# Performance work log

Measured on AMD Instinct MI355X. Metric: run time of the kernel, lower is better.

Reference implementation:

```python
import jax, jax.numpy as jnp
import numpy as np

MODEL_DIM = 256
HEADS = 8
LN_EPS = 1e-5


def layer_norm(x, gamma, beta):
    mu = jnp.mean(x, axis=-1, keepdims=True)
    var = jnp.var(x, axis=-1, keepdims=True)
    return (x - mu) * jax.lax.rsqrt(var + LN_EPS) * gamma + beta


def setup_inputs() -> dict:
    key = jax.random.key(0)
    ks = jax.random.split(key, 4)
    bs, n, d, h = 16, 1024, MODEL_DIM, HEADS
    scale = 1.0 / np.sqrt(d)
    x = jax.random.normal(ks[0], (bs, n, d), dtype=jnp.float32)
    Wq = jax.random.normal(ks[1], (d * h, d), dtype=jnp.float32) * scale
    Wk = jax.random.normal(ks[2], (d * h, d), dtype=jnp.float32) * scale
    Wv = jax.random.normal(ks[3], (d, d * h), dtype=jnp.float32) * (1.0 / np.sqrt(d * h))
    gamma = jnp.ones((d,), dtype=jnp.float32)
    beta = jnp.zeros((d,), dtype=jnp.float32)
    return {"x": x, "Wq": Wq, "Wk": Wk, "Wv": Wv, "gamma": gamma, "beta": beta}


def reference(x, Wq, Wk, Wv, gamma, beta):
    bs, n, d = x.shape
    h = HEADS
    # pre-norm
    xn = layer_norm(x, gamma, beta)
    # q, k: (bs, n, h, d) -> (bs, h, n, d); torch Linear: y = x @ W.T
    q = (xn @ Wq.T).reshape(bs, n, h, d).transpose(0, 2, 1, 3)
    k = (xn @ Wk.T).reshape(bs, n, h, d).transpose(0, 2, 1, 3)
    scores = jnp.einsum('bhid,bhjd->bhij', q, k) / jnp.sqrt(jnp.float32(d))
    probs = jax.nn.softmax(scores, axis=-1)  # dropout prob = 0.0
    # shared (non-per-head) value: V = xn broadcast over heads
    context = jnp.einsum('bhij,bjd->bhid', probs, xn)
    context = context.transpose(0, 2, 1, 3).reshape(bs, n, h * d)
    out = context @ Wv.T + xn  # residual uses post-pre-norm x (as in source when pre_norm)
    return out, probs
```

## Files before the change

### kernel.cpp

```cpp
#include <hip/hip_runtime.h>
#include <stdint.h>


typedef __bf16 bh8 __attribute__((ext_vector_type(8)));
typedef float f32x4 __attribute__((ext_vector_type(4)));

#define MFMA16(a, b, c) __builtin_amdgcn_mfma_f32_16x16x32_bf16((a), (b), (c), 0, 0, 0)

__device__ __forceinline__ uint16_t f2b(float f) {
  uint32_t u = __float_as_uint(f);
  u += 0x7FFFu + ((u >> 16) & 1u);
  return (uint16_t)(u >> 16);
}
__device__ __forceinline__ uint32_t pack2(float a, float b) {
  return (uint32_t)f2b(a) | ((uint32_t)f2b(b) << 16);
}
__device__ __forceinline__ void async16(const uint16_t* g, uint16_t* l) {
  __builtin_amdgcn_global_load_lds((__attribute__((address_space(1))) const uint32_t*)g,
                                   (__attribute__((address_space(3))) uint32_t*)l, 16, 0, 0);
}

__global__ __launch_bounds__(256) void ln_kernel(
    const float* __restrict__ x, const float* __restrict__ gamma,
    const float* __restrict__ beta, float* __restrict__ xnf, uint16_t* __restrict__ xnb) {
  const int wave = threadIdx.x >> 6, lane = threadIdx.x & 63;
  const size_t row = (size_t)blockIdx.x * 4 + wave;
  const float4 v = *(const float4*)(x + row * 256 + lane * 4);
  float s = v.x + v.y + v.z + v.w;
  float ss = v.x * v.x + v.y * v.y + v.z * v.z + v.w * v.w;
#pragma unroll
  for (int d = 32; d; d >>= 1) { s += __shfl_xor(s, d); ss += __shfl_xor(ss, d); }
  const float mu = s * (1.0f / 256.0f);
  const float inv = rsqrtf(ss * (1.0f / 256.0f) - mu * mu + 1e-5f);
  const float4 g = *(const float4*)(gamma + lane * 4);
  const float4 be = *(const float4*)(beta + lane * 4);
  float4 o;
  o.x = (v.x - mu) * inv * g.x + be.x;
  o.y = (v.y - mu) * inv * g.y + be.y;
  o.z = (v.z - mu) * inv * g.z + be.z;
  o.w = (v.w - mu) * inv * g.w + be.w;
  *(float4*)(xnf + row * 256 + lane * 4) = o;
  ushort4 ob;
  ob.x = f2b(o.x); ob.y = f2b(o.y); ob.z = f2b(o.z); ob.w = f2b(o.w);
  *(ushort4*)(xnb + row * 256 + lane * 4) = ob;
}

__global__ __launch_bounds__(256) void cvt_kernel(const float* __restrict__ in,
                                                  uint16_t* __restrict__ out2, int n) {
  int i = blockIdx.x * 256 + threadIdx.x;
  if (i < n) out2[i] = f2b(in[i]);
}

__global__ __launch_bounds__(256) void transpose_xn(
    const uint16_t* __restrict__ xnb, uint16_t* __restrict__ xnT) {
  const int b = blockIdx.z, it = blockIdx.y, dt = blockIdx.x;
  __shared__ uint16_t tile[64][65];
  const int t = threadIdx.x;
  const int r = t >> 2, c0 = (t & 3) * 16;
  const uint16_t* src = xnb + ((size_t)b * 1024 + it * 64) * 256 + dt * 64;
#pragma unroll
  for (int i = 0; i < 16; ++i) tile[r][c0 + i] = src[(size_t)r * 256 + c0 + i];
  __syncthreads();
  uint16_t* dst = xnT + ((size_t)b * 256 + dt * 64) * 1024 + it * 64;
#pragma unroll
  for (int i = 0; i < 16; ++i) dst[(size_t)r * 1024 + c0 + i] = tile[c0 + i][r];
}

template <int K, int N, bool RES>
__global__ __launch_bounds__(256) void gemm_bt(
    const uint16_t* __restrict__ A, const uint16_t* __restrict__ B,
    void* __restrict__ Cv, const float* __restrict__ resid) {
  const int m0 = blockIdx.x * 128, n0 = blockIdx.y * 128;
  const int t = threadIdx.x;
  const int lane = t & 63, wave = t >> 6;
  const int l15 = lane & 15, quad = lane >> 4;
  const int wm = (wave >> 1) * 64, wn = (wave & 1) * 64;

  __shared__ uint16_t As[128 * 32];
  __shared__ uint16_t Bs[128 * 32];

  f32x4 acc[4][4];
#pragma unroll
  for (int mi = 0; mi < 4; ++mi)
#pragma unroll
    for (int ni = 0; ni < 4; ++ni)
#pragma unroll
      for (int r = 0; r < 4; ++r) acc[mi][ni][r] = 0.0f;

  for (int k0 = 0; k0 < K; k0 += 32) {
#pragma unroll
    for (int j = 0; j < 2; ++j) {
      int cc = j * 256 + t;
      int row = cc >> 2, ko = (cc & 3) << 3;
      async16(A + (size_t)(m0 + row) * K + k0 + ko, &As[(j * 256 + (t & ~63)) * 8]);
      async16(B + (size_t)(n0 + row) * K + k0 + ko, &Bs[(j * 256 + (t & ~63)) * 8]);
    }
    __syncthreads();
    bh8 afr[4], bfr[4];
#pragma unroll
    for (int mi = 0; mi < 4; ++mi) afr[mi] = *(const bh8*)&As[(wm + mi * 16 + l15) * 32 + quad * 8];
#pragma unroll
    for (int ni = 0; ni < 4; ++ni) bfr[ni] = *(const bh8*)&Bs[(wn + ni * 16 + l15) * 32 + quad * 8];
#pragma unroll
    for (int mi = 0; mi < 4; ++mi)
#pragma unroll
      for (int ni = 0; ni < 4; ++ni) acc[mi][ni] = MFMA16(afr[mi], bfr[ni], acc[mi][ni]);
    __syncthreads();
  }
#pragma unroll
  for (int mi = 0; mi < 4; ++mi)
#pragma unroll
    for (int ni = 0; ni < 4; ++ni)
#pragma unroll
      for (int r = 0; r < 4; ++r) {
        size_t m = (size_t)(m0 + wm + mi * 16 + quad * 4 + r);
        size_t n = (size_t)(n0 + wn + ni * 16 + l15);
        if constexpr (RES) {
          ((float*)Cv)[m * N + n] = acc[mi][ni][r] + resid[m * N + n];
        } else {
          ((uint16_t*)Cv)[m * N + n] = f2b(acc[mi][ni][r]);
        }
      }
}

__global__ __launch_bounds__(256) void attn_scores(
    const uint16_t* __restrict__ Qp, const uint16_t* __restrict__ Kp,
    float* __restrict__ probs) {
  const int rb = blockIdx.x;
  const int z = blockIdx.y;
  const int b = z >> 3, h = z & 7;
  const int t = threadIdx.x;
  const int lane = t & 63, wave = t >> 6;
  const int l15 = lane & 15, quad = lane >> 4;
  const int m0 = rb * 32;

  const uint16_t* Qb = Qp + (size_t)b * 1024 * 2048 + (size_t)h * 256;
  const uint16_t* Kb = Kp + (size_t)b * 1024 * 2048 + (size_t)h * 256;

  __shared__ uint16_t As[32 * 32];
  __shared__ uint16_t Bs[512 * 32];
  __shared__ float redmax[32][4];
  __shared__ float redsum[32][4];

  f32x4 acc[2][16];
#pragma unroll
  for (int mi = 0; mi < 2; ++mi)
#pragma unroll
    for (int ni = 0; ni < 16; ++ni)
#pragma unroll
      for (int r = 0; r < 4; ++r) acc[mi][ni][r] = 0.0f;

  bh8 af[2];
  for (int k0 = 0; k0 < 256; k0 += 32) {
#pragma unroll
    for (int half = 0; half < 2; ++half) {
      if (half == 0 && t < 128) {
        int row = t >> 2, ko = (t & 3) << 3;
        async16(Qb + (size_t)(m0 + row) * 2048 + k0 + ko, &As[(t & ~63) * 8]);
      }
#pragma unroll
      for (int j = 0; j < 8; ++j) {
        int cc = j * 256 + t;
        int row = half * 512 + (cc >> 2), ko = (cc & 3) << 3;
        async16(Kb + (size_t)row * 2048 + k0 + ko, &Bs[(j * 256 + (t & ~63)) * 8]);
      }
      __syncthreads();
      if (half == 0) {
        af[0] = *(const bh8*)&As[l15 * 32 + quad * 8];
        af[1] = *(const bh8*)&As[(16 + l15) * 32 + quad * 8];
      }
#pragma unroll
      for (int ni = 0; ni < 8; ++ni) {
        bh8 bf = *(const bh8*)&Bs[(wave * 128 + ni * 16 + l15) * 32 + quad * 8];
        acc[0][half * 8 + ni] = MFMA16(af[0], bf, acc[0][half * 8 + ni]);
        acc[1][half * 8 + ni] = MFMA16(af[1], bf, acc[1][half * 8 + ni]);
      }
      __syncthreads();
    }
  }

  const float sc = 0.0625f * 1.44269504f;
  float rowm[2][4];
#pragma unroll
  for (int mi = 0; mi < 2; ++mi)
#pragma unroll
    for (int r = 0; r < 4; ++r) {
      float m = acc[mi][0][r];
#pragma unroll
      for (int ni = 1; ni < 16; ++ni) m = fmaxf(m, acc[mi][ni][r]);
#pragma unroll
      for (int d = 1; d < 16; d <<= 1) m = fmaxf(m, __shfl_xor(m, d));
      rowm[mi][r] = m;
    }
  if (l15 == 0) {
#pragma unroll
    for (int mi = 0; mi < 2; ++mi)
#pragma unroll
      for (int r = 0; r < 4; ++r) redmax[mi * 16 + quad * 4 + r][wave] = rowm[mi][r];
  }
  __syncthreads();
#pragma unroll
  for (int mi = 0; mi < 2; ++mi)
#pragma unroll
    for (int r = 0; r < 4; ++r) {
      int row = mi * 16 + quad * 4 + r;
      rowm[mi][r] = fmaxf(fmaxf(redmax[row][0], redmax[row][1]),
                          fmaxf(redmax[row][2], redmax[row][3]));
    }
  float rsum[2][4];
#pragma unroll
  for (int mi = 0; mi < 2; ++mi)
#pragma unroll
    for (int r = 0; r < 4; ++r) rsum[mi][r] = 0.0f;
#pragma unroll
  for (int mi = 0; mi < 2; ++mi)
#pragma unroll
    for (int ni = 0; ni < 16; ++ni)
#pragma unroll
      for (int r = 0; r < 4; ++r) {
        float e = exp2f((acc[mi][ni][r] - rowm[mi][r]) * sc);
        acc[mi][ni][r] = e;
        rsum[mi][r] += e;
      }
#pragma unroll
  for (int mi = 0; mi < 2; ++mi)
#pragma unroll
    for (int r = 0; r < 4; ++r) {
#pragma unroll
      for (int d = 1; d < 16; d <<= 1) rsum[mi][r] += __shfl_xor(rsum[mi][r], d);
    }
  if (l15 == 0) {
#pragma unroll
    for (int mi = 0; mi < 2; ++mi)
#pragma unroll
      for (int r = 0; r < 4; ++r) redsum[mi * 16 + quad * 4 + r][wave] = rsum[mi][r];
  }
  __syncthreads();
  float rinv[2][4];
#pragma unroll
  for (int mi = 0; mi < 2; ++mi)
#pragma unroll
    for (int r = 0; r < 4; ++r) {
      int row = mi * 16 + quad * 4 + r;
      rinv[mi][r] = 1.0f / (redsum[row][0] + redsum[row][1] + redsum[row][2] + redsum[row][3]);
    }
  float* P = probs + (size_t)z * 1024 * 1024 + (size_t)m0 * 1024;
#pragma unroll
  for (int mi = 0; mi < 2; ++mi)
#pragma unroll
    for (int ni = 0; ni < 16; ++ni)
#pragma unroll
      for (int r = 0; r < 4; ++r) {
        int row = mi * 16 + quad * 4 + r;
        int col = (ni >> 3) * 512 + wave * 128 + (ni & 7) * 16 + l15;
        P[(size_t)row * 1024 + col] = acc[mi][ni][r] * rinv[mi][r];
      }
}

__global__ __launch_bounds__(512) void gemm_ctx(
    const float* __restrict__ P, const uint16_t* __restrict__ XT,
    uint16_t* __restrict__ ctx) {
  const int mt = blockIdx.x;
  const int z = blockIdx.z;
  const int b = z >> 3, h = z & 7;
  const int t = threadIdx.x;
  const int lane = t & 63, wave = t >> 6;
  const int l15 = lane & 15, quad = lane >> 4;
  const int wm = (wave >> 2) * 64, wn = (wave & 3) * 64;
  const int m0 = mt * 128;
  const float* Ab = P + (size_t)z * 1024 * 1024;
  const uint16_t* Bb = XT + (size_t)b * 256 * 1024;

  __shared__ uint16_t As[128 * 32];
  __shared__ uint16_t Bs[256 * 32];

  f32x4 acc[4][4];
#pragma unroll
  for (int mi = 0; mi < 4; ++mi)
#pragma unroll
    for (int ni = 0; ni < 4; ++ni)
#pragma unroll
      for (int r = 0; r < 4; ++r) acc[mi][ni][r] = 0.0f;

  const int arow = t >> 2, aco = (t & 3) * 8;
  for (int k0 = 0; k0 < 1024; k0 += 32) {
    {
      const float* g = Ab + (size_t)(m0 + arow) * 1024 + k0 + aco;
      float4 f0 = *(const float4*)g;
      float4 f1 = *(const float4*)(g + 4);
      uint4 pk;
      pk.x = pack2(f0.x, f0.y); pk.y = pack2(f0.z, f0.w);
      pk.z = pack2(f1.x, f1.y); pk.w = pack2(f1.z, f1.w);
      *(uint4*)&As[arow * 32 + aco] = pk;
    }
#pragma unroll
    for (int j = 0; j < 2; ++j) {
      int cc = j * 512 + t;
      int row = cc >> 2, ko = (cc & 3) << 3;
      async16(Bb + (size_t)row * 1024 + k0 + ko, &Bs[(j * 512 + (t & ~63)) * 8]);
    }
    __syncthreads();
    bh8 afr[4], bfr[4];
#pragma unroll
    for (int mi = 0; mi < 4; ++mi) afr[mi] = *(const bh8*)&As[(wm + mi * 16 + l15) * 32 + quad * 8];
#pragma unroll
    for (int ni = 0; ni < 4; ++ni) bfr[ni] = *(const bh8*)&Bs[(wn + ni * 16 + l15) * 32 + quad * 8];
#pragma unroll
    for (int mi = 0; mi < 4; ++mi)
#pragma unroll
      for (int ni = 0; ni < 4; ++ni) acc[mi][ni] = MFMA16(afr[mi], bfr[ni], acc[mi][ni]);
    __syncthreads();
  }
  const size_t growbase = (size_t)b * 1024 + m0 + wm;
#pragma unroll
  for (int mi = 0; mi < 4; ++mi)
#pragma unroll
    for (int ni = 0; ni < 4; ++ni)
#pragma unroll
      for (int r = 0; r < 4; ++r) {
        size_t grow = growbase + mi * 16 + quad * 4 + r;
        int col = h * 256 + wn + ni * 16 + l15;
        ctx[grow * 2048 + col] = f2b(acc[mi][ni][r]);
      }
}

extern "C" void kernel_launch(void* const* d_in, const int* in_sizes, int n_in,
                              void* d_out, int out_size, void* d_ws, size_t ws_size,
                              hipStream_t stream) {
  const float* x = (const float*)d_in[0];
  const float* Wq = (const float*)d_in[1];
  const float* Wk = (const float*)d_in[2];
  const float* Wv = (const float*)d_in[3];
  const float* gamma = (const float*)d_in[4];
  const float* beta = (const float*)d_in[5];
  float* out = (float*)d_out;
  float* probs = out + (size_t)16 * 1024 * 256;

  char* ws = (char*)d_ws;
  float* xnf = (float*)(ws + 0);
  uint16_t* xnb = (uint16_t*)(ws + 16777216);
  uint16_t* xnT = (uint16_t*)(ws + 25165824);
  uint16_t* wqb = (uint16_t*)(ws + 33554432);
  uint16_t* wkb = (uint16_t*)(ws + 34603008);
  uint16_t* wvb = (uint16_t*)(ws + 35651584);
  uint16_t* Qp = (uint16_t*)(ws + 36700160);
  uint16_t* Kp = (uint16_t*)(ws + 103809024);
  uint16_t* ctx = (uint16_t*)(ws + 170917888);

  ln_kernel<<<4096, 256, 0, stream>>>(x, gamma, beta, xnf, xnb);
  cvt_kernel<<<2048, 256, 0, stream>>>(Wq, wqb, 2048 * 256);
  cvt_kernel<<<2048, 256, 0, stream>>>(Wk, wkb, 2048 * 256);
  cvt_kernel<<<2048, 256, 0, stream>>>(Wv, wvb, 256 * 2048);
  transpose_xn<<<dim3(4, 16, 16), 256, 0, stream>>>(xnb, xnT);
  gemm_bt<256, 2048, false><<<dim3(128, 16), 256, 0, stream>>>(xnb, wqb, (void*)Qp, nullptr);
  gemm_bt<256, 2048, false><<<dim3(128, 16), 256, 0, stream>>>(xnb, wkb, (void*)Kp, nullptr);
  attn_scores<<<dim3(32, 128), 256, 0, stream>>>(Qp, Kp, probs);
  gemm_ctx<<<dim3(8, 1, 128), 512, 0, stream>>>(probs, xnT, ctx);
  gemm_bt<2048, 256, true><<<dim3(128, 2), 256, 0, stream>>>(ctx, wvb, (void*)out, xnf);
}
```

Measured before the change: 1.192 ms.

## Double-buffer LDS tiles, swizzle workgroups across XCDs, and retile context GEMM

Adds double-buffered LDS staging to the projection GEMM, the score kernel and the context GEMM, so the next K-slice loads while MFMAs run on the current one. It also flattens the grids and remaps block IDs round-robin across the 8 XCDs so neighbouring tiles share L2. The score kernel now loads Q fragments straight from global memory into registers and gets an occupancy hint of 2. The context GEMM moves to 64x256 tiles with 256 threads. Doubling LDS raises per-block shared memory, which may reduce occupancy.

```diff
diff --git a/kernel.cpp b/kernel.cpp
--- a/kernel.cpp
+++ b/kernel.cpp
@@ -70,14 +70,17 @@
 __global__ __launch_bounds__(256) void gemm_bt(
     const uint16_t* __restrict__ A, const uint16_t* __restrict__ B,
     void* __restrict__ Cv, const float* __restrict__ resid) {
-  const int m0 = blockIdx.x * 128, n0 = blockIdx.y * 128;
+  const int nwg = gridDim.x, cpx = nwg >> 3;
+  const int lid = blockIdx.x;
+  const int swz = (lid & 7) * cpx + (lid >> 3);
+  const int m0 = (swz & 127) * 128, n0 = (swz >> 7) * 128;
   const int t = threadIdx.x;
   const int lane = t & 63, wave = t >> 6;
   const int l15 = lane & 15, quad = lane >> 4;
   const int wm = (wave >> 1) * 64, wn = (wave & 1) * 64;
 
-  __shared__ uint16_t As[128 * 32];
-  __shared__ uint16_t Bs[128 * 32];
+  __shared__ uint16_t As[2][128 * 32];
+  __shared__ uint16_t Bs[2][128 * 32];
 
   f32x4 acc[4][4];
 #pragma unroll
@@ -87,25 +90,34 @@
 #pragma unroll
       for (int r = 0; r < 4; ++r) acc[mi][ni][r] = 0.0f;
 
-  for (int k0 = 0; k0 < K; k0 += 32) {
+  auto stage = [&](int buf, int k0) {
 #pragma unroll
     for (int j = 0; j < 2; ++j) {
       int cc = j * 256 + t;
       int row = cc >> 2, ko = (cc & 3) << 3;
-      async16(A + (size_t)(m0 + row) * K + k0 + ko, &As[(j * 256 + (t & ~63)) * 8]);
-      async16(B + (size_t)(n0 + row) * K + k0 + ko, &Bs[(j * 256 + (t & ~63)) * 8]);
-    }
-    __syncthreads();
+      async16(A + (size_t)(m0 + row) * K + k0 + ko, &As[buf][(j * 256 + (t & ~63)) * 8]);
+      async16(B + (size_t)(n0 + row) * K + k0 + ko, &Bs[buf][(j * 256 + (t & ~63)) * 8]);
+    }
+  };
+
+  stage(0, 0);
+  __syncthreads();
+  int cur = 0;
+  for (int k0 = 0; k0 < K; k0 += 32) {
+    if (k0 + 32 < K) stage(cur ^ 1, k0 + 32);
     bh8 afr[4], bfr[4];
 #pragma unroll
-    for (int mi = 0; mi < 4; ++mi) afr[mi] = *(const bh8*)&As[(wm + mi * 16 + l15) * 32 + quad * 8];
-#pragma unroll
-    for (int ni = 0; ni < 4; ++ni) bfr[ni] = *(const bh8*)&Bs[(wn + ni * 16 + l15) * 32 + quad * 8];
+    for (int mi = 0; mi < 4; ++mi)
+      afr[mi] = *(const bh8*)&As[cur][(wm + mi * 16 + l15) * 32 + quad * 8];
+#pragma unroll
+    for (int ni = 0; ni < 4; ++ni)
+      bfr[ni] = *(const bh8*)&Bs[cur][(wn + ni * 16 + l15) * 32 + quad * 8];
 #pragma unroll
     for (int mi = 0; mi < 4; ++mi)
 #pragma unroll
       for (int ni = 0; ni < 4; ++ni) acc[mi][ni] = MFMA16(afr[mi], bfr[ni], acc[mi][ni]);
     __syncthreads();
+    cur ^= 1;
   }
 #pragma unroll
   for (int mi = 0; mi < 4; ++mi)
@@ -123,11 +135,12 @@
       }
 }
 
-__global__ __launch_bounds__(256) void attn_scores(
+__global__ __launch_bounds__(256, 2) void attn_scores(
     const uint16_t* __restrict__ Qp, const uint16_t* __restrict__ Kp,
     float* __restrict__ probs) {
-  const int rb = blockIdx.x;
-  const int z = blockIdx.y;
+  const int lid = blockIdx.x;
+  const int swz = (lid & 7) * 512 + (lid >> 3);
+  const int z = swz >> 5, rb = swz & 31;
   const int b = z >> 3, h = z & 7;
   const int t = threadIdx.x;
   const int lane = t & 63, wave = t >> 6;
@@ -137,8 +150,7 @@
   const uint16_t* Qb = Qp + (size_t)b * 1024 * 2048 + (size_t)h * 256;
   const uint16_t* Kb = Kp + (size_t)b * 1024 * 2048 + (size_t)h * 256;
 
-  __shared__ uint16_t As[32 * 32];
-  __shared__ uint16_t Bs[512 * 32];
+  __shared__ uint16_t Bs[2][512 * 32];
   __shared__ float redmax[32][4];
   __shared__ float redsum[32][4];
 
@@ -150,33 +162,43 @@
 #pragma unroll
       for (int r = 0; r < 4; ++r) acc[mi][ni][r] = 0.0f;
 
-  bh8 af[2];
-  for (int k0 = 0; k0 < 256; k0 += 32) {
-#pragma unroll
-    for (int half = 0; half < 2; ++half) {
-      if (half == 0 && t < 128) {
-        int row = t >> 2, ko = (t & 3) << 3;
-        async16(Qb + (size_t)(m0 + row) * 2048 + k0 + ko, &As[(t & ~63) * 8]);
-      }
-#pragma unroll
-      for (int j = 0; j < 8; ++j) {
-        int cc = j * 256 + t;
-        int row = half * 512 + (cc >> 2), ko = (cc & 3) << 3;
-        async16(Kb + (size_t)row * 2048 + k0 + ko, &Bs[(j * 256 + (t & ~63)) * 8]);
-      }
-      __syncthreads();
-      if (half == 0) {
-        af[0] = *(const bh8*)&As[l15 * 32 + quad * 8];
-        af[1] = *(const bh8*)&As[(16 + l15) * 32 + quad * 8];
-      }
-#pragma unroll
-      for (int ni = 0; ni < 8; ++ni) {
-        bh8 bf = *(const bh8*)&Bs[(wave * 128 + ni * 16 + l15) * 32 + quad * 8];
-        acc[0][half * 8 + ni] = MFMA16(af[0], bf, acc[0][half * 8 + ni]);
-        acc[1][half * 8 + ni] = MFMA16(af[1], bf, acc[1][half * 8 + ni]);
-      }
-      __syncthreads();
-    }
+  auto stageB = [&](int buf, int p) {
+    const int k0 = (p >> 1) * 32, half = p & 1;
+#pragma unroll
+    for (int j = 0; j < 8; ++j) {
+      int cc = j * 256 + t;
+      int row = half * 512 + (cc >> 2), ko = (cc & 3) << 3;
+      async16(Kb + (size_t)row * 2048 + k0 + ko, &Bs[buf][(j * 256 + (t & ~63)) * 8]);
+    }
+  };
+
+  bh8 aq[2][2];
+#pragma unroll
+  for (int mi = 0; mi < 2; ++mi)
+    aq[0][mi] = *(const bh8*)(Qb + (size_t)(m0 + mi * 16 + l15) * 2048 + quad * 8);
+
+  stageB(0, 0);
+  __syncthreads();
+
+  int cur = 0;
+#pragma unroll
+  for (int p = 0; p < 16; ++p) {
+    const int ks = p >> 1, half = p & 1;
+    if (half == 0 && ks < 7) {
+#pragma unroll
+      for (int mi = 0; mi < 2; ++mi)
+        aq[(ks + 1) & 1][mi] =
+            *(const bh8*)(Qb + (size_t)(m0 + mi * 16 + l15) * 2048 + (ks + 1) * 32 + quad * 8);
+    }
+    if (p < 15) stageB(cur ^ 1, p + 1);
+#pragma unroll
+    for (int ni = 0; ni < 8; ++ni) {
+      bh8 bf = *(const bh8*)&Bs[cur][(wave * 128 + ni * 16 + l15) * 32 + quad * 8];
+      acc[0][half * 8 + ni] = MFMA16(aq[ks & 1][0], bf, acc[0][half * 8 + ni]);
+      acc[1][half * 8 + ni] = MFMA16(aq[ks & 1][1], bf, acc[1][half * 8 + ni]);
+    }
+    __syncthreads();
+    cur ^= 1;
   }
 
   const float sc = 0.0625f * 1.44269504f;
@@ -257,65 +279,89 @@
       }
 }
 
-__global__ __launch_bounds__(512) void gemm_ctx(
+__global__ __launch_bounds__(256) void gemm_ctx(
     const float* __restrict__ P, const uint16_t* __restrict__ XT,
     uint16_t* __restrict__ ctx) {
-  const int mt = blockIdx.x;
-  const int z = blockIdx.z;
+  const int lid = blockIdx.x;
+  const int swz = (lid & 7) * 256 + (lid >> 3);
+  const int z = swz >> 4, mt = swz & 15;
   const int b = z >> 3, h = z & 7;
   const int t = threadIdx.x;
   const int lane = t & 63, wave = t >> 6;
   const int l15 = lane & 15, quad = lane >> 4;
-  const int wm = (wave >> 2) * 64, wn = (wave & 3) * 64;
-  const int m0 = mt * 128;
+  const int wm = (wave >> 1) * 32, wn = (wave & 1) * 128;
+  const int m0 = mt * 64;
   const float* Ab = P + (size_t)z * 1024 * 1024;
   const uint16_t* Bb = XT + (size_t)b * 256 * 1024;
 
-  __shared__ uint16_t As[128 * 32];
-  __shared__ uint16_t Bs[256 * 32];
-
-  f32x4 acc[4][4];
-#pragma unroll
-  for (int mi = 0; mi < 4; ++mi)
-#pragma unroll
-    for (int ni = 0; ni < 4; ++ni)
+  __shared__ uint16_t As[2][64 * 32];
+  __shared__ uint16_t Bs[2][256 * 32];
+
+  f32x4 acc[2][8];
+#pragma unroll
+  for (int mi = 0; mi < 2; ++mi)
+#pragma unroll
+    for (int ni = 0; ni < 8; ++ni)
 #pragma unroll
       for (int r = 0; r < 4; ++r) acc[mi][ni][r] = 0.0f;
 
   const int arow = t >> 2, aco = (t & 3) * 8;
+  const float* ag = Ab + (size_t)(m0 + arow) * 1024 + aco;
+
+  auto stageB = [&](int buf, int k0) {
+#pragma unroll
+    for (int j = 0; j < 4; ++j) {
+      int cc = j * 256 + t;
+      int row = cc >> 2, ko = (cc & 3) << 3;
+      async16(Bb + (size_t)row * 1024 + k0 + ko, &Bs[buf][(j * 256 + (t & ~63)) * 8]);
+    }
+  };
+
+  {
+    float4 f0 = *(const float4*)(ag);
+    float4 f1 = *(const float4*)(ag + 4);
+    stageB(0, 0);
+    uint4 pk;
+    pk.x = pack2(f0.x, f0.y); pk.y = pack2(f0.z, f0.w);
+    pk.z = pack2(f1.x, f1.y); pk.w = pack2(f1.z, f1.w);
+    *(uint4*)&As[0][arow * 32 + aco] = pk;
+  }
+  __syncthreads();
+
+  int cur = 0;
   for (int k0 = 0; k0 < 1024; k0 += 32) {
-    {
-      const float* g = Ab + (size_t)(m0 + arow) * 1024 + k0 + aco;
-      float4 f0 = *(const float4*)g;
-      float4 f1 = *(const float4*)(g + 4);
+    const bool nxt = (k0 + 32) < 1024;
+    float4 g0, g1;
+    if (nxt) {
+      g0 = *(const float4*)(ag + k0 + 32);
+      g1 = *(const float4*)(ag + k0 + 36);
+    }
+    if (nxt) stageB(cur ^ 1, k0 + 32);
+    bh8 afr[2], bfr[8];
+#pragma unroll
+    for (int mi = 0; mi < 2; ++mi)
+      afr[mi] = *(const bh8*)&As[cur][(wm + mi * 16 + l15) * 32 + quad * 8];
+#pragma unroll
+    for (int ni = 0; ni < 8; ++ni)
+      bfr[ni] = *(const bh8*)&Bs[cur][(wn + ni * 16 + l15) * 32 + quad * 8];
+#pragma unroll
+    for (int mi = 0; mi < 2; ++mi)
+#pragma unroll
+      for (int ni = 0; ni < 8; ++ni) acc[mi][ni] = MFMA16(afr[mi], bfr[ni], acc[mi][ni]);
+    if (nxt) {
       uint4 pk;
-      pk.x = pack2(f0.x, f0.y); pk.y = pack2(f0.z, f0.w);
-      pk.z = pack2(f1.x, f1.y); pk.w = pack2(f1.z, f1.w);
-      *(uint4*)&As[arow * 32 + aco] = pk;
-    }
-#pragma unroll
-    for (int j = 0; j < 2; ++j) {
-      int cc = j * 512 + t;
-      int row = cc >> 2, ko = (cc & 3) << 3;
-      async16(Bb + (size_t)row * 1024 + k0 + ko, &Bs[(j * 512 + (t & ~63)) * 8]);
+      pk.x = pack2(g0.x, g0.y); pk.y = pack2(g0.z, g0.w);
+      pk.z = pack2(g1.x, g1.y); pk.w = pack2(g1.z, g1.w);
+      *(uint4*)&As[cur ^ 1][arow * 32 + aco] = pk;
     }
     __syncthreads();
-    bh8 afr[4], bfr[4];
-#pragma unroll
-    for (int mi = 0; mi < 4; ++mi) afr[mi] = *(const bh8*)&As[(wm + mi * 16 + l15) * 32 + quad * 8];
-#pragma unroll
-    for (int ni = 0; ni < 4; ++ni) bfr[ni] = *(const bh8*)&Bs[(wn + ni * 16 + l15) * 32 + quad * 8];
-#pragma unroll
-    for (int mi = 0; mi < 4; ++mi)
-#pragma unroll
-      for (int ni = 0; ni < 4; ++ni) acc[mi][ni] = MFMA16(afr[mi], bfr[ni], acc[mi][ni]);
-    __syncthreads();
+    cur ^= 1;
   }
   const size_t growbase = (size_t)b * 1024 + m0 + wm;
 #pragma unroll
-  for (int mi = 0; mi < 4; ++mi)
-#pragma unroll
-    for (int ni = 0; ni < 4; ++ni)
+  for (int mi = 0; mi < 2; ++mi)
+#pragma unroll
+    for (int ni = 0; ni < 8; ++ni)
 #pragma unroll
       for (int r = 0; r < 4; ++r) {
         size_t grow = growbase + mi * 16 + quad * 4 + r;
@@ -352,9 +398,9 @@
   cvt_kernel<<<2048, 256, 0, stream>>>(Wk, wkb, 2048 * 256);
   cvt_kernel<<<2048, 256, 0, stream>>>(Wv, wvb, 256 * 2048);
   transpose_xn<<<dim3(4, 16, 16), 256, 0, stream>>>(xnb, xnT);
-  gemm_bt<256, 2048, false><<<dim3(128, 16), 256, 0, stream>>>(xnb, wqb, (void*)Qp, nullptr);
-  gemm_bt<256, 2048, false><<<dim3(128, 16), 256, 0, stream>>>(xnb, wkb, (void*)Kp, nullptr);
-  attn_scores<<<dim3(32, 128), 256, 0, stream>>>(Qp, Kp, probs);
-  gemm_ctx<<<dim3(8, 1, 128), 512, 0, stream>>>(probs, xnT, ctx);
-  gemm_bt<2048, 256, true><<<dim3(128, 2), 256, 0, stream>>>(ctx, wvb, (void*)out, xnf);
-}
+  gemm_bt<256, 2048, false><<<2048, 256, 0, stream>>>(xnb, wqb, (void*)Qp, nullptr);
+  gemm_bt<256, 2048, false><<<2048, 256, 0, stream>>>(xnb, wkb, (void*)Kp, nullptr);
+  attn_scores<<<4096, 256, 0, stream>>>(Qp, Kp, probs);
+  gemm_ctx<<<2048, 256, 0, stream>>>(probs, xnT, ctx);
+  gemm_bt<2048, 256, true><<<256, 256, 0, stream>>>(ctx, wvb, (void*)out, xnf);
+}
```

After: 1.121 ms. 1.06x faster.
